# Optimization experiments

Measured on AMD Instinct MI355X. Metric: run time of the kernel, lower is better.

Reference implementation:

```python
import jax, jax.numpy as jnp
import numpy as np
from jax import lax

B, T, N, FIN = 1, 8, 50000, 3
E = 800000
HID, HEADS = 32, 2
NEG_SLOPE = 0.2  # PyG GATConv default negative_slope


def setup_inputs() -> dict:
    key = jax.random.key(0)
    ks = jax.random.split(key, 16)
    p = lambda k, shape: jax.random.normal(k, shape, dtype=jnp.float32) * 0.1
    return {
        "x_seq": jax.random.normal(ks[0], (B, T, N, FIN), dtype=jnp.float32),
        # GAT layer 1: lin weight [heads*hid, in], att vectors [heads, hid], bias [hid]
        "W1": p(ks[1], (HEADS * HID, FIN)),
        "a1_src": p(ks[2], (HEADS, HID)),
        "a1_dst": p(ks[3], (HEADS, HID)),
        "b1": p(ks[4], (HID,)),
        # GAT layer 2
        "W2": p(ks[5], (HEADS * HID, HID)),
        "a2_src": p(ks[6], (HEADS, HID)),
        "a2_dst": p(ks[7], (HEADS, HID)),
        "b2": p(ks[8], (HID,)),
        # GRU (single layer): torch layout [3*hid, hid] with gate order r,z,n
        "w_ih": p(ks[9], (3 * HID, HID)),
        "w_hh": p(ks[10], (3 * HID, HID)),
        "b_ih": p(ks[11], (3 * HID,)),
        "b_hh": p(ks[12], (3 * HID,)),
        # final Linear(hid, 1)
        "fc_w": p(ks[13], (1, HID)),
        "fc_b": p(ks[14], (1,)),
        "edge_index": jax.random.randint(ks[15], (2, E), 0, N, dtype=jnp.int64),
    }


def gat(x, src, dst, W, a_s, a_d, b):
    """PyG GATConv, heads=HEADS, concat=False (mean over heads). src/dst include self-loops."""
    n = x.shape[0]
    heads, hd = a_s.shape
    h = (x @ W.T).reshape(n, heads, hd)                      # [n, heads, hid]
    e = jax.nn.leaky_relu((h * a_s).sum(-1)[src] + (h * a_d).sum(-1)[dst], NEG_SLOPE)  # [E', heads]
    m = jax.ops.segment_max(e, dst, num_segments=n)          # per-destination max
    m = jnp.where(jnp.isfinite(m), m, jnp.zeros_like(m))
    ex = jnp.exp(e - m[dst])
    denom = jax.ops.segment_sum(ex, dst, num_segments=n)
    alpha = ex / (denom[dst] + 1e-16)                        # segment softmax
    out = jax.ops.segment_sum(h[src] * alpha[..., None], dst, num_segments=n)  # [n, heads, hid]
    return out.mean(axis=1) + b


def _forward(x_seq, W1, a1_src, a1_dst, b1, W2, a2_src, a2_dst, b2,
             w_ih, w_hh, b_ih, b_hh, fc_w, fc_b, edge_index):
    Bb, Tt, Nn, Fin = x_seq.shape
    n = Bb * Nn
    loops = jnp.arange(n, dtype=edge_index.dtype)            # add_self_loops=True
    src = jnp.concatenate([edge_index[0], loops])
    dst = jnp.concatenate([edge_index[1], loops])
    hid = b1.shape[0]

    def step(hstate, xt):                                    # one timestep: GAT x2 then GRU cell
        x = xt.reshape(n, Fin)
        g = jax.nn.relu(gat(x, src, dst, W1, a1_src, a1_dst, b1))
        g = jax.nn.relu(gat(g, src, dst, W2, a2_src, a2_dst, b2))
        gi = g @ w_ih.T + b_ih
        gh = hstate @ w_hh.T + b_hh
        i_r, i_z, i_n = jnp.split(gi, 3, axis=-1)
        h_r, h_z, h_n = jnp.split(gh, 3, axis=-1)
        r = jax.nn.sigmoid(i_r + h_r)
        z = jax.nn.sigmoid(i_z + h_z)
        cand = jnp.tanh(i_n + r * h_n)
        hnew = (1.0 - z) * cand + z * hstate
        return hnew, None

    h0 = jnp.zeros((n, hid), x_seq.dtype)
    h_final, _ = lax.scan(step, h0, jnp.moveaxis(x_seq, 1, 0))  # scan over T
    out = h_final @ fc_w.T + fc_b                            # [B*N, 1]
    return out.reshape(Bb, Nn)


def reference(x_seq, W1, a1_src, a1_dst, b1, W2, a2_src, a2_dst, b2,
              w_ih, w_hh, b_ih, b_hh, fc_w, fc_b, edge_index):
    return _forward(x_seq, W1, a1_src, a1_dst, b1, W2, a2_src, a2_dst, b2,
                    w_ih, w_hh, b_ih, b_hh, fc_w, fc_b, edge_index)
```

## Files before the change

kernel.cpp:

```cpp
#include <hip/hip_runtime.h>
#include <hip/hip_fp16.h>
#include <stdint.h>

#define T_STEPS 8
#define FIN 3
#define HID 32
#define NEG_SLOPE 0.2f
#define LOG2E 1.4426950408889634f

typedef __fp16 v4h __attribute__((ext_vector_type(4)));
typedef __fp16 v2h __attribute__((ext_vector_type(2)));
typedef float  v4f __attribute__((ext_vector_type(4)));

__device__ __forceinline__ float lrelu(float x) { return x > 0.f ? x : NEG_SLOPE * x; }
__device__ __forceinline__ float sigmoidf(float x) { return 1.f / (1.f + __expf(-x)); }

__device__ __forceinline__ float fdot2h(__half2 a, __half2 b, float c) {
#if __has_builtin(__builtin_amdgcn_fdot2)
    union { __half2 h; v2h v; } ua, ub;
    ua.h = a; ub.h = b;
    return __builtin_amdgcn_fdot2(ua.v, ub.v, c, false);
#else
    float2 fa = __half22float2(a), fb = __half22float2(b);
    return c + fa.x * fb.x + fa.y * fb.y;
#endif
}

__global__ void detect_kernel(const int* ei32, int nElems, int* flag) {
    __shared__ int any_nonzero;
    if (threadIdx.x == 0) any_nonzero = 0;
    __syncthreads();
    int idx = 1 + 2 * (int)threadIdx.x;
    if (idx < nElems && ei32[idx] != 0) any_nonzero = 1;
    __syncthreads();
    if (threadIdx.x == 0) *flag = (any_nonzero ? 0 : 1);
}

__device__ __forceinline__ int get_edge(const void* ei, int is64, long long idx) {
    if (is64) return (int)((const long long*)ei)[idx];
    return ((const int*)ei)[idx];
}

__global__ void init_kernel(int* cnt, int N) {
    int i = blockIdx.x * 256 + threadIdx.x;
    if (i < N) cnt[i] = 1;
}

__global__ void conv_count_kernel(const void* ei, const int* flag, int E, int N,
                                  int* src32, int* dst32, int* cnt) {
    int e = blockIdx.x * 256 + threadIdx.x;
    if (e >= E) return;
    int is64 = *flag;
    int s = get_edge(ei, is64, e);
    int d = get_edge(ei, is64, (long long)E + e);
    if ((unsigned)s >= (unsigned)N) s = 0;
    src32[e] = s;
    int dd = ((unsigned)d < (unsigned)N) ? d : 0x7fffffff;
    dst32[e] = dd;
    if (dd < N) atomicAdd(&cnt[dd], 1);
}

__global__ __launch_bounds__(256) void scan1_kernel(const int* cnt, int* rowptr, int* bsum, int n) {
    __shared__ int sm[256];
    int i = blockIdx.x * 256 + threadIdx.x;
    int v = (i < n) ? cnt[i] : 0;
    sm[threadIdx.x] = v;
    __syncthreads();
    for (int off = 1; off < 256; off <<= 1) {
        int t = (threadIdx.x >= off) ? sm[threadIdx.x - off] : 0;
        __syncthreads();
        sm[threadIdx.x] += t;
        __syncthreads();
    }
    if (i < n) rowptr[i + 1] = sm[threadIdx.x];
    if (threadIdx.x == 255) bsum[blockIdx.x] = sm[255];
}

__global__ __launch_bounds__(256) void scan2_kernel(int* bsum, int nb) {
    __shared__ int sm[256];
    int v = (threadIdx.x < nb) ? bsum[threadIdx.x] : 0;
    sm[threadIdx.x] = v;
    __syncthreads();
    for (int off = 1; off < 256; off <<= 1) {
        int t = (threadIdx.x >= off) ? sm[threadIdx.x - off] : 0;
        __syncthreads();
        sm[threadIdx.x] += t;
        __syncthreads();
    }
    if (threadIdx.x < nb) bsum[threadIdx.x] = sm[threadIdx.x];
}

__global__ __launch_bounds__(256) void scan3_kernel(int* rowptr, const int* bsum, int n) {
    int i = blockIdx.x * 256 + threadIdx.x;
    if (i < n && blockIdx.x > 0) rowptr[i + 1] += bsum[blockIdx.x - 1];
    if (i == 0) rowptr[0] = 0;
}

__global__ void selffill_kernel(const int* rowptr, int* csr, int* fill, int N) {
    int n = blockIdx.x * 256 + threadIdx.x;
    if (n >= N) return;
    int rp = rowptr[n];
    csr[rp] = n;
    fill[n] = rp + 1;
}

__global__ void scatter_kernel(const int* __restrict__ src32, const int* __restrict__ dst32,
                               int E, int lo, int hi, int* fill, int* csr) {
    int e = blockIdx.x * 256 + threadIdx.x;
    if (e >= E) return;
    int d = dst32[e];
    if (d < lo || d >= hi) return;
    int p = atomicAdd(&fill[d], 1);
    csr[p] = src32[e];
}

__global__ __launch_bounds__(64) void prep_u_kernel(
        const float* __restrict__ W2, const float* __restrict__ a2s,
        const float* __restrict__ a2d, float* __restrict__ u_s, float* __restrict__ u_d) {
    int l = threadIdx.x;
    int h = l >> 5, k = l & 31;
    float us = 0.f, ud = 0.f;
    for (int c = 0; c < 32; c++) {
        float w = W2[(h * 32 + c) * 32 + k];
        us += a2s[h * 32 + c] * w;
        ud += a2d[h * 32 + c] * w;
    }
    u_s[l] = us * LOG2E;
    u_d[l] = ud * LOG2E;
}

__global__ __launch_bounds__(256) void pack_kernel(
        const float* __restrict__ W2, __half2* __restrict__ w2h) {
    int idx = blockIdx.x * 256 + threadIdx.x;
    if (idx >= 1024) return;
    int kp = idx >> 6, r = idx & 63;
    float a = 0.5f * W2[r * 32 + 2 * kp];
    float b = 0.5f * W2[r * 32 + 2 * kp + 1];
    w2h[idx] = __floats2half2_rn(a, b);
}

__global__ __launch_bounds__(256) void packfrag_kernel(
        const float* __restrict__ w_ih, const float* __restrict__ w_hh,
        uint2* __restrict__ wfrag) {
    int idx = blockIdx.x * 256 + threadIdx.x;
    if (idx >= 1536) return;
    int q24 = idx >> 6, l = idx & 63;
    int c = l & 15, g = l >> 4;
    const float* W = (q24 < 12) ? w_ih : w_hh;
    int q = (q24 < 12) ? q24 : q24 - 12;
    int nt = q >> 1, kt = q & 1;
    float v[4];
#pragma unroll
    for (int b = 0; b < 4; b++) {
        int kk = kt * 16 + 4 * g + b;
        int nn = nt * 16 + c;
        v[b] = W[nn * 32 + kk];
    }
    __half2 lo = __floats2half2_rn(v[0], v[1]);
    __half2 hi = __floats2half2_rn(v[2], v[3]);
    uint2 u;
    u.x = *(unsigned*)&lo;
    u.y = *(unsigned*)&hi;
    wfrag[(8 + q24) * 64 + l] = u;
}

__global__ __launch_bounds__(256) void score1_all(
        const float* __restrict__ x_seq, const float* __restrict__ W1,
        const float* __restrict__ a1s, const float* __restrict__ a1d,
        float4* __restrict__ nrec4, float2* __restrict__ sd1, int N) {
    int t = blockIdx.x;
    int node = blockIdx.y * 256 + threadIdx.x;
    if (node >= N) return;
    const float* xp = x_seq + ((size_t)t * N + node) * FIN;
    float x0 = xp[0], x1 = xp[1], x2 = xp[2];
    float ps0 = 0.f, ps1 = 0.f, pd0 = 0.f, pd1 = 0.f;
    for (int c = 0; c < 32; c++) {
        float h0 = W1[c * 3] * x0 + W1[c * 3 + 1] * x1 + W1[c * 3 + 2] * x2;
        float h1 = W1[96 + c * 3] * x0 + W1[97 + c * 3] * x1 + W1[98 + c * 3] * x2;
        ps0 += h0 * a1s[c]; pd0 += h0 * a1d[c];
        ps1 += h1 * a1s[32 + c]; pd1 += h1 * a1d[32 + c];
    }
    ps0 *= LOG2E; ps1 *= LOG2E; pd0 *= LOG2E; pd1 *= LOG2E;
    unsigned u = (unsigned)__half_as_ushort(__float2half_rn(ps0)) |
                 ((unsigned)__half_as_ushort(__float2half_rn(ps1)) << 16);
    float4 r;
    r.x = x0; r.y = x1; r.z = x2; r.w = __uint_as_float(u);
    nrec4[(size_t)t * N + node] = r;
    sd1[(size_t)t * N + node] = make_float2(pd0, pd1);
}

__device__ __forceinline__ void unpack_scores(float wslot, float& s0, float& s1) {
    unsigned u = __float_as_uint(wslot);
    s0 = __half2float(__ushort_as_half((unsigned short)(u & 0xffffu)));
    s1 = __half2float(__ushort_as_half((unsigned short)(u >> 16)));
}

__global__ __launch_bounds__(64) void aggA_all(
        const int* __restrict__ rowptr, const int* __restrict__ csr,
        const float4* __restrict__ nrec4, const float2* __restrict__ sd1,
        const float* __restrict__ W1, const float* __restrict__ b1,
        const float* __restrict__ u_s, const float* __restrict__ u_d,
        __half2* __restrict__ g1h, float2* __restrict__ ssd2, float2* __restrict__ sd2, int N) {
    int t = blockIdx.x;
    int dst = blockIdx.y * 64 + threadIdx.x;
    if (dst >= N) return;
    const float4* nr = nrec4 + (size_t)t * N;
    int rs = rowptr[dst], re = rowptr[dst + 1];
    float2 sdv = sd1[(size_t)t * N + dst];
    float q0 = 0, qx0 = 0, qx1 = 0, qx2 = 0;
    float q1 = 0, qy0 = 0, qy1 = 0, qy2 = 0;
#define AGGA_EDGE(rr) { \
        float s0h, s1h; unpack_scores(rr.w, s0h, s1h); \
        float w0 = exp2f(lrelu(s0h + sdv.x)); \
        float w1 = exp2f(lrelu(s1h + sdv.y)); \
        q0 += w0; qx0 += w0 * rr.x; qx1 += w0 * rr.y; qx2 += w0 * rr.z; \
        q1 += w1; qy0 += w1 * rr.x; qy1 += w1 * rr.y; qy2 += w1 * rr.z; }
    int e = rs;
    for (; e + 4 <= re; e += 4) {
        int s0 = csr[e], s1 = csr[e + 1], s2 = csr[e + 2], s3 = csr[e + 3];
        float4 r0 = nr[s0], r1 = nr[s1], r2 = nr[s2], r3 = nr[s3];
        AGGA_EDGE(r0); AGGA_EDGE(r1); AGGA_EDGE(r2); AGGA_EDGE(r3);
    }
    for (; e < re; e++) {
        float4 r = nr[csr[e]];
        AGGA_EDGE(r);
    }
#undef AGGA_EDGE
    float inv0 = 1.f / (q0 + 1e-16f), inv1 = 1.f / (q1 + 1e-16f);
    float ax0 = qx0 * inv0, ax1 = qx1 * inv0, ax2 = qx2 * inv0;
    float ay0 = qy0 * inv1, ay1 = qy1 * inv1, ay2 = qy2 * inv1;
    float ps0 = 0, ps1 = 0, pd0 = 0, pd1 = 0;
    float4 out[4];
    __half2* ghp = (__half2*)out;
    float gprev = 0.f;
#pragma unroll
    for (int c = 0; c < 32; c++) {
        float v0 = W1[c * 3] * ax0 + W1[c * 3 + 1] * ax1 + W1[c * 3 + 2] * ax2;
        float v1 = W1[96 + c * 3] * ay0 + W1[97 + c * 3] * ay1 + W1[98 + c * 3] * ay2;
        float g = fmaxf(0.5f * (v0 + v1) + b1[c], 0.f);
        ps0 += g * u_s[c];      ps1 += g * u_s[32 + c];
        pd0 += g * u_d[c];      pd1 += g * u_d[32 + c];
        if (c & 1) ghp[c >> 1] = __floats2half2_rn(gprev, g);
        else gprev = g;
    }
    float4* gdst = (float4*)(g1h + (size_t)t * N * 16 + (size_t)dst * 16);
    gdst[0] = out[0]; gdst[1] = out[1]; gdst[2] = out[2]; gdst[3] = out[3];
    ssd2[(size_t)t * N + dst] = make_float2(ps0, ps1);
    sd2[(size_t)t * N + dst]  = make_float2(pd0, pd1);
}

__global__ __launch_bounds__(256) void aggBg2_all(
        const int* __restrict__ rowptr, const int* __restrict__ csr,
        const __half2* __restrict__ g1h,
        const float2* __restrict__ ssd2, const float2* __restrict__ sd2,
        const __half2* __restrict__ w2h, const float* __restrict__ b2,
        __half2* __restrict__ g2H, int N) {
    int t = blockIdx.x;
    int dst = blockIdx.y * 256 + threadIdx.x;
    if (dst >= N) return;
    const __half2* gt = g1h + (size_t)t * N * 16;
    const float2* ss = ssd2 + (size_t)t * N;
    int rs = rowptr[dst], re = rowptr[dst + 1];
    float2 sdv = sd2[(size_t)t * N + dst];
    float den0 = 0.f, den1 = 0.f;
    float a0f[32], a1f[32];
#pragma unroll
    for (int j = 0; j < 32; j++) { a0f[j] = 0.f; a1f[j] = 0.f; }
    union Row { float4 f[4]; __half2 h[16]; };
#define AGGB_EDGE(sc, rr) { \
        float w0 = exp2f(lrelu(sc.x + sdv.x)); \
        float w1 = exp2f(lrelu(sc.y + sdv.y)); \
        den0 += w0; den1 += w1; \
        __half2 w0h = __float2half2_rn(w0); \
        __half2 w1h = __float2half2_rn(w1); \
        _Pragma("unroll") \
        for (int j = 0; j < 16; j++) { \
            p0[j] = __hfma2(w0h, rr.h[j], p0[j]); \
            p1[j] = __hfma2(w1h, rr.h[j], p1[j]); \
        } }
    int e = rs;
    while (e < re) {
        int lim = min(re, e + 16);
        __half2 p0[16], p1[16];
        __half2 z = __floats2half2_rn(0.f, 0.f);
#pragma unroll
        for (int j = 0; j < 16; j++) { p0[j] = z; p1[j] = z; }
        for (; e + 2 <= lim; e += 2) {
            int s0 = csr[e], s1 = csr[e + 1];
            float2 c0 = ss[s0], c1 = ss[s1];
            const float4* r0p = (const float4*)(gt + (size_t)s0 * 16);
            const float4* r1p = (const float4*)(gt + (size_t)s1 * 16);
            Row r0, r1;
            r0.f[0] = r0p[0]; r0.f[1] = r0p[1]; r0.f[2] = r0p[2]; r0.f[3] = r0p[3];
            r1.f[0] = r1p[0]; r1.f[1] = r1p[1]; r1.f[2] = r1p[2]; r1.f[3] = r1p[3];
            AGGB_EDGE(c0, r0);
            AGGB_EDGE(c1, r1);
        }
        for (; e < lim; e++) {
            int s = csr[e];
            float2 c = ss[s];
            const float4* rp = (const float4*)(gt + (size_t)s * 16);
            Row r;
            r.f[0] = rp[0]; r.f[1] = rp[1]; r.f[2] = rp[2]; r.f[3] = rp[3];
            AGGB_EDGE(c, r);
        }
#pragma unroll
        for (int j = 0; j < 16; j++) {
            float2 v0 = __half22float2(p0[j]);
            float2 v1 = __half22float2(p1[j]);
            a0f[2 * j] += v0.x; a0f[2 * j + 1] += v0.y;
            a1f[2 * j] += v1.x; a1f[2 * j + 1] += v1.y;
        }
    }
#undef AGGB_EDGE
    float i0 = 1.f / (den0 + 1e-16f), i1 = 1.f / (den1 + 1e-16f);
    __half2 an0[16], an1[16];
#pragma unroll
    for (int j = 0; j < 16; j++) {
        an0[j] = __floats2half2_rn(a0f[2 * j] * i0, a0f[2 * j + 1] * i0);
        an1[j] = __floats2half2_rn(a1f[2 * j] * i1, a1f[2 * j + 1] * i1);
    }
    __half2 og[16];
#pragma unroll
    for (int cp = 0; cp < 16; cp++) {
        float accA = 0.f, accB = 0.f;
#pragma unroll
        for (int kp = 0; kp < 16; kp++) {
            accA = fdot2h(an0[kp], w2h[kp * 64 + 2 * cp], accA);
            accA = fdot2h(an1[kp], w2h[kp * 64 + 32 + 2 * cp], accA);
            accB = fdot2h(an0[kp], w2h[kp * 64 + 2 * cp + 1], accB);
            accB = fdot2h(an1[kp], w2h[kp * 64 + 32 + 2 * cp + 1], accB);
        }
        float ga = fmaxf(accA + b2[2 * cp], 0.f);
        float gb = fmaxf(accB + b2[2 * cp + 1], 0.f);
        og[cp] = __floats2half2_rn(ga, gb);
    }
    float4* o = (float4*)(g2H + ((size_t)t * N + dst) * 16);
    o[0] = ((float4*)og)[0];
    o[1] = ((float4*)og)[1];
    o[2] = ((float4*)og)[2];
    o[3] = ((float4*)og)[3];
}

__global__ __launch_bounds__(64) void gru_mfma(
        const __half2* __restrict__ g2H, const uint2* __restrict__ wfrag,
        const float* __restrict__ b_ih, const float* __restrict__ b_hh,
        const float* __restrict__ fc_w, const float* __restrict__ fc_b,
        float* __restrict__ out, int N) {
    __shared__ __align__(16) __half h_lds[16 * 36];
    int l = threadIdx.x;
    int c = l & 15;
    int g4 = l >> 4;
    int node0 = blockIdx.x * 16;
    union FU { uint2 u; v4h h; };
    v4h Bih[6][2], Bhh[6][2];
#pragma unroll
    for (int nt = 0; nt < 6; nt++)
#pragma unroll
        for (int kt = 0; kt < 2; kt++) {
            FU f; f.u = wfrag[(8 + nt * 2 + kt) * 64 + l]; Bih[nt][kt] = f.h;
            f.u = wfrag[(20 + nt * 2 + kt) * 64 + l]; Bhh[nt][kt] = f.h;
        }
    float bir0 = b_ih[c], bir1 = b_ih[c + 16];
    float biz0 = b_ih[32 + c], biz1 = b_ih[48 + c];
    float bin0 = b_ih[64 + c], bin1 = b_ih[80 + c];
    float bhr0 = b_hh[c], bhr1 = b_hh[c + 16];
    float bhz0 = b_hh[32 + c], bhz1 = b_hh[48 + c];
    float bhn0 = b_hh[64 + c], bhn1 = b_hh[80 + c];
    float fcw0 = fc_w[c], fcw1 = fc_w[c + 16];
    v4f hold0 = {0.f, 0.f, 0.f, 0.f};
    v4f hold1 = {0.f, 0.f, 0.f, 0.f};
    const __half2* rowb = g2H + (size_t)(node0 + c) * 16;
    for (int t = 0; t < T_STEPS; t++) {
        const __half2* rb = rowb + (size_t)t * N * 16;
        v4f Di[6], Dh[6];
#pragma unroll
        for (int nt = 0; nt < 6; nt++) { Di[nt] = {0.f, 0.f, 0.f, 0.f}; Dh[nt] = {0.f, 0.f, 0.f, 0.f}; }
#pragma unroll
        for (int kt = 0; kt < 2; kt++) {
            FU Ag; Ag.u = *(const uint2*)(rb + 2 * g4 + 8 * kt);
#pragma unroll
            for (int nt = 0; nt < 6; nt++)
                Di[nt] = __builtin_amdgcn_mfma_f32_16x16x16f16(Ag.h, Bih[nt][kt], Di[nt], 0, 0, 0);
        }
        if (t > 0) {
#pragma unroll
            for (int kt = 0; kt < 2; kt++) {
                FU Ah; Ah.u = *(const uint2*)&h_lds[c * 36 + 4 * g4 + 16 * kt];
#pragma unroll
                for (int nt = 0; nt < 6; nt++)
                    Dh[nt] = __builtin_amdgcn_mfma_f32_16x16x16f16(Ah.h, Bhh[nt][kt], Dh[nt], 0, 0, 0);
            }
        }
        v4f hn0, hn1;
#pragma unroll
        for (int i = 0; i < 4; i++) {
            {
                float rr = sigmoidf((Di[0][i] + bir0) + (Dh[0][i] + bhr0));
                float zz = sigmoidf((Di[2][i] + biz0) + (Dh[2][i] + bhz0));
                float cand = tanhf((Di[4][i] + bin0) + rr * (Dh[4][i] + bhn0));
                hn0[i] = (1.f - zz) * cand + zz * hold0[i];
            }
            {
                float rr = sigmoidf((Di[1][i] + bir1) + (Dh[1][i] + bhr1));
                float zz = sigmoidf((Di[3][i] + biz1) + (Dh[3][i] + bhz1));
                float cand = tanhf((Di[5][i] + bin1) + rr * (Dh[5][i] + bhn1));
                hn1[i] = (1.f - zz) * cand + zz * hold1[i];
            }
        }
        hold0 = hn0; hold1 = hn1;
        if (t < T_STEPS - 1) {
            __syncthreads();
#pragma unroll
            for (int i = 0; i < 4; i++) {
                int nrow = 4 * g4 + i;
                h_lds[nrow * 36 + c]      = __float2half_rn(hn0[i]);
                h_lds[nrow * 36 + c + 16] = __float2half_rn(hn1[i]);
            }
            __syncthreads();
        }
    }
#pragma unroll
    for (int i = 0; i < 4; i++) {
        float p = fcw0 * hold0[i] + fcw1 * hold1[i];
        p += __shfl_xor(p, 1, 64);
        p += __shfl_xor(p, 2, 64);
        p += __shfl_xor(p, 4, 64);
        p += __shfl_xor(p, 8, 64);
        if (c == 0) out[node0 + 4 * g4 + i] = p + fc_b[0];
    }
}

extern "C" void kernel_launch(void* const* d_in, const int* in_sizes, int n_in,
                              void* d_out, int out_size, void* d_ws, size_t ws_size,
                              hipStream_t stream) {
    const float* x_seq = (const float*)d_in[0];
    const float* W1  = (const float*)d_in[1];
    const float* a1s = (const float*)d_in[2];
    const float* a1d = (const float*)d_in[3];
    const float* b1  = (const float*)d_in[4];
    const float* W2  = (const float*)d_in[5];
    const float* a2s = (const float*)d_in[6];
    const float* a2d = (const float*)d_in[7];
    const float* b2  = (const float*)d_in[8];
    const float* w_ih = (const float*)d_in[9];
    const float* w_hh = (const float*)d_in[10];
    const float* b_ih = (const float*)d_in[11];
    const float* b_hh = (const float*)d_in[12];
    const float* fc_w = (const float*)d_in[13];
    const float* fc_b = (const float*)d_in[14];
    const void*  ei   = d_in[15];

    const int N = in_sizes[0] / (T_STEPS * FIN);
    const int E = in_sizes[15] / 2;
    const int NE = E + N;
    const int NB = (N + 255) / 256;
    const int NB64 = (N + 63) / 64;
    const int NB16 = (N + 15) / 16;
    const int EB = (E + 255) / 256;

    char* ws = (char*)d_ws;
    size_t off = 0;
    auto alloc = [&](size_t bytes) -> void* {
        void* p = ws + off;
        off += (bytes + 255) & ~(size_t)255;
        return p;
    };
    int*     flag   = (int*)alloc(4);
    int*     rowptr = (int*)alloc((size_t)(N + 1) * 4);
    int*     cnt    = (int*)alloc((size_t)N * 4);
    int*     bsum   = (int*)alloc(256 * 4);
    int*     csr    = (int*)alloc((size_t)NE * 4);
    int*     src32  = (int*)alloc((size_t)E * 4);
    int*     dst32  = (int*)alloc((size_t)E * 4);
    float4*  nrec4  = (float4*)alloc((size_t)T_STEPS * N * 16);
    float2*  sd1    = (float2*)alloc((size_t)T_STEPS * N * 8);
    float2*  ssd2   = (float2*)alloc((size_t)T_STEPS * N * 8);
    float2*  sd2    = (float2*)alloc((size_t)T_STEPS * N * 8);
    __half2* g1h    = (__half2*)alloc((size_t)T_STEPS * N * 16 * 4);
    __half2* g2H    = (__half2*)alloc((size_t)T_STEPS * N * 16 * 4);
    float*   u_s    = (float*)alloc(64 * 4);
    float*   u_d    = (float*)alloc(64 * 4);
    __half2* w2h    = (__half2*)alloc(1024 * 4);
    uint2*   wfrag  = (uint2*)alloc(32 * 64 * 8);
    if (off > ws_size) return;

    detect_kernel<<<1, 128, 0, stream>>>((const int*)ei, in_sizes[15], flag);
    init_kernel<<<NB, 256, 0, stream>>>(cnt, N);
    conv_count_kernel<<<EB, 256, 0, stream>>>(ei, flag, E, N, src32, dst32, cnt);
    scan1_kernel<<<NB, 256, 0, stream>>>(cnt, rowptr, bsum, N);
    scan2_kernel<<<1, 256, 0, stream>>>(bsum, NB);
    scan3_kernel<<<NB, 256, 0, stream>>>(rowptr, bsum, N);
    selffill_kernel<<<NB, 256, 0, stream>>>(rowptr, csr, cnt, N);
    {
        const int NPASS = 2;
        int per = (N + NPASS - 1) / NPASS;
        for (int p = 0; p < NPASS; p++) {
            int lo = p * per;
            int hi = min(lo + per, N);
            scatter_kernel<<<EB, 256, 0, stream>>>(src32, dst32, E, lo, hi, cnt, csr);
        }
    }
    prep_u_kernel<<<1, 64, 0, stream>>>(W2, a2s, a2d, u_s, u_d);
    pack_kernel<<<4, 256, 0, stream>>>(W2, w2h);
    packfrag_kernel<<<6, 256, 0, stream>>>(w_ih, w_hh, wfrag);

    score1_all<<<dim3(T_STEPS, NB), 256, 0, stream>>>(x_seq, W1, a1s, a1d, nrec4, sd1, N);
    aggA_all<<<dim3(T_STEPS, NB64), 64, 0, stream>>>(rowptr, csr, nrec4, sd1, W1, b1,
                                                     u_s, u_d, g1h, ssd2, sd2, N);
    aggBg2_all<<<dim3(T_STEPS, NB), 256, 0, stream>>>(rowptr, csr, g1h, ssd2, sd2,
                                                      w2h, b2, g2H, N);
    gru_mfma<<<NB16, 64, 0, stream>>>(g2H, wfrag, b_ih, b_hh,
                                      fc_w, fc_b, (float*)d_out, N);
}
```

Baseline: 321.5 us.

## Split aggBg2 per-node work across two lanes with shuffle exchange

```diff
diff --git a/kernel.cpp b/kernel.cpp
--- a/kernel.cpp
+++ b/kernel.cpp
@@ -256,17 +256,19 @@
         const __half2* __restrict__ w2h, const float* __restrict__ b2,
         __half2* __restrict__ g2H, int N) {
     int t = blockIdx.x;
-    int dst = blockIdx.y * 256 + threadIdx.x;
+    int tid = threadIdx.x;
+    int dst = blockIdx.y * 128 + (tid >> 1);
+    int q = tid & 1;
     if (dst >= N) return;
-    const __half2* gt = g1h + (size_t)t * N * 16;
+    const __half2* gt = g1h + (size_t)t * N * 16 + q * 8;
     const float2* ss = ssd2 + (size_t)t * N;
     int rs = rowptr[dst], re = rowptr[dst + 1];
     float2 sdv = sd2[(size_t)t * N + dst];
     float den0 = 0.f, den1 = 0.f;
-    float a0f[32], a1f[32];
-#pragma unroll
-    for (int j = 0; j < 32; j++) { a0f[j] = 0.f; a1f[j] = 0.f; }
-    union Row { float4 f[4]; __half2 h[16]; };
+    float a0f[16], a1f[16];
+#pragma unroll
+    for (int j = 0; j < 16; j++) { a0f[j] = 0.f; a1f[j] = 0.f; }
+    union Half { float4 f[2]; __half2 h[8]; };
 #define AGGB_EDGE(sc, rr) { \
         float w0 = exp2f(lrelu(sc.x + sdv.x)); \
         float w1 = exp2f(lrelu(sc.y + sdv.y)); \
@@ -274,25 +276,25 @@
         __half2 w0h = __float2half2_rn(w0); \
         __half2 w1h = __float2half2_rn(w1); \
         _Pragma("unroll") \
-        for (int j = 0; j < 16; j++) { \
+        for (int j = 0; j < 8; j++) { \
             p0[j] = __hfma2(w0h, rr.h[j], p0[j]); \
             p1[j] = __hfma2(w1h, rr.h[j], p1[j]); \
         } }
     int e = rs;
     while (e < re) {
         int lim = min(re, e + 16);
-        __half2 p0[16], p1[16];
+        __half2 p0[8], p1[8];
         __half2 z = __floats2half2_rn(0.f, 0.f);
 #pragma unroll
-        for (int j = 0; j < 16; j++) { p0[j] = z; p1[j] = z; }
+        for (int j = 0; j < 8; j++) { p0[j] = z; p1[j] = z; }
         for (; e + 2 <= lim; e += 2) {
             int s0 = csr[e], s1 = csr[e + 1];
             float2 c0 = ss[s0], c1 = ss[s1];
             const float4* r0p = (const float4*)(gt + (size_t)s0 * 16);
             const float4* r1p = (const float4*)(gt + (size_t)s1 * 16);
-            Row r0, r1;
-            r0.f[0] = r0p[0]; r0.f[1] = r0p[1]; r0.f[2] = r0p[2]; r0.f[3] = r0p[3];
-            r1.f[0] = r1p[0]; r1.f[1] = r1p[1]; r1.f[2] = r1p[2]; r1.f[3] = r1p[3];
+            Half r0, r1;
+            r0.f[0] = r0p[0]; r0.f[1] = r0p[1];
+            r1.f[0] = r1p[0]; r1.f[1] = r1p[1];
             AGGB_EDGE(c0, r0);
             AGGB_EDGE(c1, r1);
         }
@@ -300,12 +302,12 @@
             int s = csr[e];
             float2 c = ss[s];
             const float4* rp = (const float4*)(gt + (size_t)s * 16);
-            Row r;
-            r.f[0] = rp[0]; r.f[1] = rp[1]; r.f[2] = rp[2]; r.f[3] = rp[3];
+            Half r;
+            r.f[0] = rp[0]; r.f[1] = rp[1];
             AGGB_EDGE(c, r);
         }
 #pragma unroll
-        for (int j = 0; j < 16; j++) {
+        for (int j = 0; j < 8; j++) {
             float2 v0 = __half22float2(p0[j]);
             float2 v1 = __half22float2(p1[j]);
             a0f[2 * j] += v0.x; a0f[2 * j + 1] += v0.y;
@@ -314,32 +316,46 @@
     }
 #undef AGGB_EDGE
     float i0 = 1.f / (den0 + 1e-16f), i1 = 1.f / (den1 + 1e-16f);
-    __half2 an0[16], an1[16];
-#pragma unroll
-    for (int j = 0; j < 16; j++) {
+    __half2 an0[8], an1[8];
+#pragma unroll
+    for (int j = 0; j < 8; j++) {
         an0[j] = __floats2half2_rn(a0f[2 * j] * i0, a0f[2 * j + 1] * i0);
         an1[j] = __floats2half2_rn(a1f[2 * j] * i1, a1f[2 * j + 1] * i1);
     }
-    __half2 og[16];
-#pragma unroll
-    for (int cp = 0; cp < 16; cp++) {
+    __half2 f0[16], f1[16];
+#pragma unroll
+    for (int j = 0; j < 8; j++) {
+        unsigned o0 = __shfl_xor(*(unsigned*)&an0[j], 1, 64);
+        unsigned o1 = __shfl_xor(*(unsigned*)&an1[j], 1, 64);
+        __half2 oh0 = *(__half2*)&o0;
+        __half2 oh1 = *(__half2*)&o1;
+        if (q == 0) {
+            f0[j] = an0[j]; f0[8 + j] = oh0;
+            f1[j] = an1[j]; f1[8 + j] = oh1;
+        } else {
+            f0[j] = oh0; f0[8 + j] = an0[j];
+            f1[j] = oh1; f1[8 + j] = an1[j];
+        }
+    }
+    __half2 og[8];
+#pragma unroll
+    for (int cp8 = 0; cp8 < 8; cp8++) {
+        int cpg = q * 8 + cp8;
         float accA = 0.f, accB = 0.f;
 #pragma unroll
         for (int kp = 0; kp < 16; kp++) {
-            accA = fdot2h(an0[kp], w2h[kp * 64 + 2 * cp], accA);
-            accA = fdot2h(an1[kp], w2h[kp * 64 + 32 + 2 * cp], accA);
-            accB = fdot2h(an0[kp], w2h[kp * 64 + 2 * cp + 1], accB);
-            accB = fdot2h(an1[kp], w2h[kp * 64 + 32 + 2 * cp + 1], accB);
-        }
-        float ga = fmaxf(accA + b2[2 * cp], 0.f);
-        float gb = fmaxf(accB + b2[2 * cp + 1], 0.f);
-        og[cp] = __floats2half2_rn(ga, gb);
-    }
-    float4* o = (float4*)(g2H + ((size_t)t * N + dst) * 16);
+            accA = fdot2h(f0[kp], w2h[kp * 64 + 2 * cpg], accA);
+            accA = fdot2h(f1[kp], w2h[kp * 64 + 32 + 2 * cpg], accA);
+            accB = fdot2h(f0[kp], w2h[kp * 64 + 2 * cpg + 1], accB);
+            accB = fdot2h(f1[kp], w2h[kp * 64 + 32 + 2 * cpg + 1], accB);
+        }
+        float ga = fmaxf(accA + b2[2 * cpg], 0.f);
+        float gb = fmaxf(accB + b2[2 * cpg + 1], 0.f);
+        og[cp8] = __floats2half2_rn(ga, gb);
+    }
+    float4* o = (float4*)(g2H + ((size_t)t * N + dst) * 16 + q * 8);
     o[0] = ((float4*)og)[0];
     o[1] = ((float4*)og)[1];
-    o[2] = ((float4*)og)[2];
-    o[3] = ((float4*)og)[3];
 }
 
 __global__ __launch_bounds__(64) void gru_mfma(
@@ -456,6 +472,7 @@
     const int NE = E + N;
     const int NB = (N + 255) / 256;
     const int NB64 = (N + 63) / 64;
+    const int NB128 = (N + 127) / 128;
     const int NB16 = (N + 15) / 16;
     const int EB = (E + 255) / 256;
 
@@ -508,8 +525,8 @@
     score1_all<<<dim3(T_STEPS, NB), 256, 0, stream>>>(x_seq, W1, a1s, a1d, nrec4, sd1, N);
     aggA_all<<<dim3(T_STEPS, NB64), 64, 0, stream>>>(rowptr, csr, nrec4, sd1, W1, b1,
                                                      u_s, u_d, g1h, ssd2, sd2, N);
-    aggBg2_all<<<dim3(T_STEPS, NB), 256, 0, stream>>>(rowptr, csr, g1h, ssd2, sd2,
-                                                      w2h, b2, g2H, N);
+    aggBg2_all<<<dim3(T_STEPS, NB128), 256, 0, stream>>>(rowptr, csr, g1h, ssd2, sd2,
+                                                         w2h, b2, g2H, N);
     gru_mfma<<<NB16, 64, 0, stream>>>(g2H, wfrag, b_ih, b_hh,
                                       fc_w, fc_b, (float*)d_out, N);
 }
```

Result: no change. 324.9 us (+1.1%).
